# Kernel tuning notes

Measured on AMD Instinct MI355X. Metric: run time of the kernel, lower is better.

The kernel has to match this reference:

```python
import math
import jax, jax.numpy as jnp
import numpy as np

B, L, H, E = 16, 2048, 8, 64
FACTOR = 1


def setup_inputs() -> dict:
    key = jax.random.key(0)
    kq, kk, kv = jax.random.split(key, 3)
    queries = jax.random.normal(kq, (B, L, H, E), dtype=jnp.float32)
    keys = jax.random.normal(kk, (B, L, H, E), dtype=jnp.float32)
    values = jax.random.normal(kv, (B, L, H, E), dtype=jnp.float32)
    return {"queries": queries, "keys": keys, "values": values, "attn_mask": 0}


def reference(queries, keys, values, attn_mask):
    # queries/keys/values: [B, L, H, E]; attn_mask is unused (as in the original).
    b, l, h, e = queries.shape
    # [B, H, E, L]
    qp = jnp.transpose(queries, (0, 2, 3, 1))
    kp = jnp.transpose(keys, (0, 2, 3, 1))
    vp = jnp.transpose(values, (0, 2, 3, 1))

    # Period-based dependency discovery via FFT cross-correlation.
    qf = jnp.fft.rfft(qp, axis=-1)
    kf = jnp.fft.rfft(kp, axis=-1)
    corr = jnp.fft.irfft(qf * jnp.conj(kf), n=l, axis=-1)  # [B, H, E, L]

    # Inference-style time-delay aggregation (per-batch top-k delays).
    top_k = max(1, int(FACTOR * math.log(l)))
    mean_value = corr.mean(axis=(1, 2))  # [B, L]
    weights, delay = jax.lax.top_k(mean_value, top_k)  # [B, K]
    tmp_corr = jax.nn.softmax(weights, axis=-1)  # [B, K]

    # Gather from doubled tensor == circular roll: index (t + delay) mod L.
    idx = (jnp.arange(l)[None, None, :] + delay[:, :, None]) % l  # [B, K, L]
    # vp[:, None]: [B, 1, H, E, L]; idx broadcast to [B, K, 1, 1, L]
    pattern = jnp.take_along_axis(vp[:, None], idx[:, :, None, None, :], axis=-1)  # [B, K, H, E, L]
    agg = jnp.einsum('bkhel,bk->bhel', pattern, tmp_corr)  # [B, H, E, L]

    return jnp.transpose(agg, (0, 3, 1, 2))  # [B, L, H, E]
```

## Files before the change

### kernel.cpp

```cpp
#include <hip/hip_runtime.h>
#include <hip/hip_fp16.h>
#include <cstdint>
#include <cstddef>

#define BB 16
#define LL 2048
#define CC 512
#define TK 7
#define PDC(a) ((a) + ((a) >> 4))
#define PSTR 1056

typedef float2 cf;
typedef __attribute__((ext_vector_type(4))) float f32x4v;

__device__ inline cf cadd(cf a, cf b){ return make_float2(a.x + b.x, a.y + b.y); }
__device__ inline cf csub(cf a, cf b){ return make_float2(a.x - b.x, a.y - b.y); }
__device__ inline cf cmul(cf a, cf b){ return make_float2(a.x*b.x - a.y*b.y, a.x*b.y + a.y*b.x); }

template<int S> __device__ inline cf crot(cf z){
  return (S < 0) ? make_float2(z.y, -z.x) : make_float2(-z.y, z.x);
}

template<int S> __device__ inline void dft4(cf* x){
  const cf t0 = cadd(x[0], x[2]), t1 = csub(x[0], x[2]);
  const cf t2 = cadd(x[1], x[3]), t3 = csub(x[1], x[3]);
  const cf r = crot<S>(t3);
  x[0] = cadd(t0, t2); x[2] = csub(t0, t2);
  x[1] = cadd(t1, r);  x[3] = csub(t1, r);
}

template<int S> __device__ inline void dft8(cf* x){
  cf e[4] = { x[0], x[2], x[4], x[6] };
  cf o[4] = { x[1], x[3], x[5], x[7] };
  dft4<S>(e); dft4<S>(o);
  const float H = 0.70710678118654752440f;
  o[1] = cmul(o[1], make_float2(H, (float)S * H));
  o[2] = crot<S>(o[2]);
  o[3] = cmul(o[3], make_float2(-H, (float)S * H));
  x[0] = cadd(e[0], o[0]); x[4] = csub(e[0], o[0]);
  x[1] = cadd(e[1], o[1]); x[5] = csub(e[1], o[1]);
  x[2] = cadd(e[2], o[2]); x[6] = csub(e[2], o[2]);
  x[3] = cadd(e[3], o[3]); x[7] = csub(e[3], o[3]);
}

struct Tw { cf w2[7], w3[7], w4a[3], w4b[3]; };

template<int S>
__device__ inline void make_tw(int tid, Tw& T){
  const float base = (float)S * 6.283185307179586f / 2048.0f;
  const int j7 = tid & 7, j63 = tid & 63;
#pragma unroll
  for (int i = 0; i < 7; ++i){
    float s, c;
    __sincosf(base * (float)(32 * (i + 1) * j7), &s, &c);  T.w2[i] = make_float2(c, s);
    __sincosf(base * (float)( 4 * (i + 1) * j63), &s, &c); T.w3[i] = make_float2(c, s);
  }
#pragma unroll
  for (int i = 0; i < 3; ++i){
    float s, c;
    __sincosf(base * (float)((i + 1) * tid), &s, &c);         T.w4a[i] = make_float2(c, s);
    __sincosf(base * (float)((i + 1) * (tid + 256)), &s, &c); T.w4b[i] = make_float2(c, s);
  }
}

template<int S>
__device__ inline void fft_s123(cf* x, cf* Bc, cf* Cc, const Tw& T, int tid){
  dft8<S>(x);
#pragma unroll
  for (int t = 0; t < 8; ++t) Bc[PDC((tid << 3) + t)] = x[t];
  __syncthreads();
  {
    cf y[8];
#pragma unroll
    for (int t = 0; t < 8; ++t) y[t] = Bc[PDC(tid + (t << 8))];
#pragma unroll
    for (int t = 1; t < 8; ++t) y[t] = cmul(y[t], T.w2[t - 1]);
    dft8<S>(y);
    const int base = ((tid >> 3) << 6) + (tid & 7);
#pragma unroll
    for (int t = 0; t < 8; ++t) Cc[PDC(base + (t << 3))] = y[t];
  }
  __syncthreads();
  {
    cf y[8];
#pragma unroll
    for (int t = 0; t < 8; ++t) y[t] = Cc[PDC(tid + (t << 8))];
#pragma unroll
    for (int t = 1; t < 8; ++t) y[t] = cmul(y[t], T.w3[t - 1]);
    dft8<S>(y);
    const int base = ((tid >> 6) << 9) + (tid & 63);
#pragma unroll
    for (int t = 0; t < 8; ++t) Bc[PDC(base + (t << 6))] = y[t];
  }
  __syncthreads();
}

__global__ __launch_bounds__(256) void transpose_pack(const float* __restrict__ q,
                                                      const float* __restrict__ k,
                                                      __half2* __restrict__ z){
  int bid = blockIdx.x;
  const int tt = bid & 31; bid >>= 5;
  const int ct = bid & 7;  bid >>= 3;
  const int b = bid;
  const int t0 = tt << 6, c0 = ct << 6;
  __shared__ __half2 T[64][69];
  const int tid = threadIdx.x;
  const size_t inbase = ((size_t)b * LL + t0) * CC + c0;
  const int c4 = (tid & 15) << 2;
  f32x4v a[4], e[4];
#pragma unroll
  for (int p2 = 0; p2 < 4; ++p2){
    const int row = (p2 << 4) + (tid >> 4);
    a[p2] = __builtin_nontemporal_load(
        reinterpret_cast<const f32x4v*>(q + inbase + (size_t)row * CC + c4));
    e[p2] = __builtin_nontemporal_load(
        reinterpret_cast<const f32x4v*>(k + inbase + (size_t)row * CC + c4));
  }
#pragma unroll
  for (int p2 = 0; p2 < 4; ++p2){
    const int row = (p2 << 4) + (tid >> 4);
    T[row][c4 + 0] = __floats2half2_rn(a[p2][0], e[p2][0]);
    T[row][c4 + 1] = __floats2half2_rn(a[p2][1], e[p2][1]);
    T[row][c4 + 2] = __floats2half2_rn(a[p2][2], e[p2][2]);
    T[row][c4 + 3] = __floats2half2_rn(a[p2][3], e[p2][3]);
  }
  __syncthreads();
  const size_t outbase = ((size_t)b * CC + c0) * LL + (size_t)t0;
#pragma unroll
  for (int it = 0; it < 4; ++it){
    const int idx = (it << 8) + tid;
    const int c = idx >> 4;
    const int t4 = (idx & 15) << 2;
    const __half2 u0 = T[t4 + 0][c], u1 = T[t4 + 1][c];
    const __half2 u2 = T[t4 + 2][c], u3 = T[t4 + 3][c];
    uint4 w;
    w.x = *reinterpret_cast<const uint*>(&u0);
    w.y = *reinterpret_cast<const uint*>(&u1);
    w.z = *reinterpret_cast<const uint*>(&u2);
    w.w = *reinterpret_cast<const uint*>(&u3);
    *reinterpret_cast<uint4*>(&z[outbase + (size_t)c * LL + t4]) = w;
  }
}

__global__ __launch_bounds__(256) void fft_fwd(const __half2* __restrict__ z,
                                               float2* __restrict__ Ppart){
  int bid = blockIdx.x;
  const int g = bid & 63; const int b = bid >> 6;
  const int tid = threadIdx.x;
  __shared__ cf Bc[2176];
  __shared__ cf Cc[2176];
  Tw T; make_tw<-1>(tid, T);
  const __half2* zg = z + (((size_t)b * CC + (size_t)g * 8) << 11);
  float accRe[4] = {0,0,0,0};
  float accIm[4] = {0,0,0,0};
  float acc1024 = 0.f;
  __half2 h[8];
#pragma unroll
  for (int t = 0; t < 8; ++t) h[t] = zg[tid + (t << 8)];
  for (int ch = 0; ch < 8; ++ch){
    cf x[8];
#pragma unroll
    for (int t = 0; t < 8; ++t) x[t] = __half22float2(h[t]);
    if (ch < 7){
      const __half2* zn = zg + ((size_t)(ch + 1) << 11);
#pragma unroll
      for (int t = 0; t < 8; ++t) h[t] = zn[tid + (t << 8)];
    }
    fft_s123<-1>(x, Bc, Cc, T, tid);
    cf y0[4], y1[4];
#pragma unroll
    for (int t = 0; t < 4; ++t) y0[t] = Bc[PDC(tid + (t << 9))];
#pragma unroll
    for (int t = 0; t < 4; ++t) y1[t] = Bc[PDC(tid + 256 + (t << 9))];
#pragma unroll
    for (int t = 1; t < 4; ++t){
      y0[t] = cmul(y0[t], T.w4a[t - 1]);
      y1[t] = cmul(y1[t], T.w4b[t - 1]);
    }
    dft4<-1>(y0); dft4<-1>(y1);
#pragma unroll
    for (int t = 0; t < 4; ++t) Cc[PDC(tid + (t << 9))] = y0[t];
#pragma unroll
    for (int t = 0; t < 4; ++t) Cc[PDC(tid + 256 + (t << 9))] = y1[t];
    __syncthreads();
    const cf Areg[4] = { y0[0], y1[0], y0[1], y1[1] };
#pragma unroll
    for (int r = 0; r < 4; ++r){
      const int f = tid + (r << 8);
      const int p = (2048 - f) & 2047;
      const cf A = Areg[r];
      const cf Bv = Cc[PDC(p)];
      accRe[r] += 0.5f  * (Bv.y * A.x + Bv.x * A.y);
      accIm[r] += 0.25f * (A.x * A.x + A.y * A.y - Bv.x * Bv.x - Bv.y * Bv.y);
    }
    if (tid == 0){
      const cf A = y0[2];
      acc1024 += A.x * A.y;
    }
  }
  float2* pp = Ppart + ((size_t)b * 64 + g) * PSTR;
#pragma unroll
  for (int r = 0; r < 4; ++r)
    pp[tid + (r << 8)] = make_float2(accRe[r], accIm[r]);
  if (tid == 0) pp[1024] = make_float2(acc1024, 0.f);
}

__global__ __launch_bounds__(256) void reduce_P(const float2* __restrict__ Ppart,
                                                float2* __restrict__ P){
  const int gid = blockIdx.x * 256 + threadIdx.x;
  const int b = gid >> 11, f = gid & 2047;
  const int src = (f <= 1024) ? f : 2048 - f;
  const float sgn = (f <= 1024) ? 1.f : -1.f;
  float sr = 0.f, si = 0.f;
#pragma unroll 8
  for (int g = 0; g < 64; ++g){
    const float2 v = Ppart[((size_t)b * 64 + g) * PSTR + src];
    sr += v.x; si += v.y;
  }
  P[((size_t)b << 11) + f] = make_float2(sr, sgn * si);
}

__global__ __launch_bounds__(256) void fft_inv_topk(const float2* __restrict__ P,
                                                    int* __restrict__ delays,
                                                    float* __restrict__ probs){
  const int b = blockIdx.x;
  const int tid = threadIdx.x;
  __shared__ cf Bc[2176];
  __shared__ cf Cc[2176];
  __shared__ float vals[2048];
  __shared__ float rv[256]; __shared__ int ri[256];
  __shared__ float wsel[TK]; __shared__ int dsel[TK];
  Tw T; make_tw<1>(tid, T);
  cf x[8];
#pragma unroll
  for (int t = 0; t < 8; ++t) x[t] = P[((size_t)b << 11) + tid + (t << 8)];
  fft_s123<1>(x, Bc, Cc, T, tid);
  const float scale = 1.0f / (2048.0f * 512.0f);
  {
#pragma unroll
    for (int hh = 0; hh < 2; ++hh){
      const int j = tid + (hh << 8);
      cf y[4];
#pragma unroll
      for (int t = 0; t < 4; ++t) y[t] = Bc[PDC(j + (t << 9))];
      const cf* w = hh ? T.w4b : T.w4a;
#pragma unroll
      for (int t = 1; t < 4; ++t) y[t] = cmul(y[t], w[t - 1]);
      dft4<1>(y);
#pragma unroll
      for (int t = 0; t < 4; ++t) vals[j + (t << 9)] = y[t].x * scale;
    }
  }
  __syncthreads();
  for (int kk = 0; kk < TK; ++kk){
    float best = -1e30f; int bi = LL;
    for (int i = tid; i < LL; i += 256){
      const float xv = vals[i];
      if (xv > best){ best = xv; bi = i; }
    }
    rv[tid] = best; ri[tid] = bi;
    __syncthreads();
    for (int s = 128; s > 0; s >>= 1){
      if (tid < s){
        const float ov = rv[tid + s]; const int oi = ri[tid + s];
        if (ov > rv[tid] || (ov == rv[tid] && oi < ri[tid])){ rv[tid] = ov; ri[tid] = oi; }
      }
      __syncthreads();
    }
    if (tid == 0){ wsel[kk] = rv[0]; dsel[kk] = ri[0]; vals[ri[0]] = -1e30f; }
    __syncthreads();
  }
  if (tid == 0){
    const float m = wsel[0];
    float e[TK], ssum = 0.f;
#pragma unroll
    for (int i = 0; i < TK; ++i){ e[i] = expf(wsel[i] - m); ssum += e[i]; }
    const float inv = 1.0f / ssum;
#pragma unroll
    for (int i = 0; i < TK; ++i){
      probs[b * TK + i] = e[i] * inv;
      delays[b * TK + i] = dsel[i];
    }
  }
}

__global__ __launch_bounds__(256) void agg_out(const float* __restrict__ v,
                                               const int* __restrict__ delays,
                                               const float* __restrict__ probs,
                                               float* __restrict__ out){
  const int bid = blockIdx.x;
  const int xcd = bid & 7;
  const int w = bid >> 3;
  const int b = (xcd << 1) + (w >> 9);
  const int local = w & 511;
  const int tid = threadIdx.x;
  const int t = (local << 2) + (tid >> 6);
  const int i0 = tid & 63;
  const int row = (b << 11) + t;
  f32x4v acc0 = {0.f, 0.f, 0.f, 0.f};
  f32x4v acc1 = {0.f, 0.f, 0.f, 0.f};
#pragma unroll
  for (int kk = 0; kk < TK; ++kk){
    const int d = delays[b * TK + kk];
    const float p = probs[b * TK + kk];
    const int srcr = (t + d) & (LL - 1);
    const size_t base = (size_t)((b << 11) + srcr) * 128;
    const f32x4v x0 = reinterpret_cast<const f32x4v*>(v)[base + i0];
    const f32x4v x1 = reinterpret_cast<const f32x4v*>(v)[base + i0 + 64];
    acc0 += x0 * p;
    acc1 += x1 * p;
  }
  f32x4v* o = reinterpret_cast<f32x4v*>(out) + (size_t)row * 128;
  o[i0] = acc0;
  o[i0 + 64] = acc1;
}

extern "C" void kernel_launch(void* const* d_in, const int* in_sizes, int n_in,
                              void* d_out, int out_size, void* d_ws, size_t ws_size,
                              hipStream_t stream){
  const float* q = (const float*)d_in[0];
  const float* k = (const float*)d_in[1];
  const float* v = (const float*)d_in[2];
  float* out = (float*)d_out;

  char* ws = (char*)d_ws;
  const size_t Z_BYTES  = (size_t)BB * CC * LL * sizeof(__half2);
  const size_t PP_BYTES = (size_t)BB * 64 * PSTR * sizeof(float2);
  const size_t P_BYTES  = (size_t)BB * LL * sizeof(float2);
  __half2* zbuf = (__half2*)ws;
  float2* Ppart = (float2*)(ws + Z_BYTES);
  float2* Pbuf  = (float2*)(ws + Z_BYTES + PP_BYTES);
  int* delays = (int*)(ws + Z_BYTES + PP_BYTES + P_BYTES);
  float* probs = (float*)(ws + Z_BYTES + PP_BYTES + P_BYTES + 1024);

  hipLaunchKernelGGL(transpose_pack, dim3(BB * 32 * 8), dim3(256), 0, stream, q, k, zbuf);
  hipLaunchKernelGGL(fft_fwd, dim3(BB * 64), dim3(256), 0, stream, zbuf, Ppart);
  hipLaunchKernelGGL(reduce_P, dim3((BB * LL) / 256), dim3(256), 0, stream, Ppart, Pbuf);
  hipLaunchKernelGGL(fft_inv_topk, dim3(BB), dim3(256), 0, stream, Pbuf, delays, probs);
  hipLaunchKernelGGL(agg_out, dim3(BB * 512), dim3(256), 0, stream,
                     v, delays, probs, out);
}
```

Before: 121.0 us.

## Split forward FFT across more blocks with single shared buffer; batch agg loads

The forward FFT kernel now launches twice as many blocks, each handling 4 channel pairs instead of 8, and uses one shared-memory buffer instead of two. This adds extra barriers so the buffer can be reused safely. The partial-sum buffer and the reduce kernel are widened to match. The aggregation kernel issues all seven gathered loads before accumulating and writes its output with nontemporal stores. The aim is more occupancy and memory-level parallelism, at the cost of a larger partial-sum reduction and more synchronisation.

```diff
diff --git a/kernel.cpp b/kernel.cpp
--- a/kernel.cpp
+++ b/kernel.cpp
@@ -9,6 +9,7 @@
 #define TK 7
 #define PDC(a) ((a) + ((a) >> 4))
 #define PSTR 1056
+#define NG 128
 
 typedef float2 cf;
 typedef __attribute__((ext_vector_type(4))) float f32x4v;
@@ -64,7 +65,7 @@
 }
 
 template<int S>
-__device__ inline void fft_s123(cf* x, cf* Bc, cf* Cc, const Tw& T, int tid){
+__device__ inline void fft_s123(cf* Bc, cf* Cc, cf* x, const Tw& T, int tid){
   dft8<S>(x);
 #pragma unroll
   for (int t = 0; t < 8; ++t) Bc[PDC((tid << 3) + t)] = x[t];
@@ -145,33 +146,61 @@
 __global__ __launch_bounds__(256) void fft_fwd(const __half2* __restrict__ z,
                                                float2* __restrict__ Ppart){
   int bid = blockIdx.x;
-  const int g = bid & 63; const int b = bid >> 6;
+  const int g = bid & (NG - 1); const int b = bid >> 7;
   const int tid = threadIdx.x;
-  __shared__ cf Bc[2176];
-  __shared__ cf Cc[2176];
+  __shared__ cf B[2176];
   Tw T; make_tw<-1>(tid, T);
-  const __half2* zg = z + (((size_t)b * CC + (size_t)g * 8) << 11);
+  const __half2* zg = z + (((size_t)b * CC + (size_t)g * 4) << 11);
   float accRe[4] = {0,0,0,0};
   float accIm[4] = {0,0,0,0};
   float acc1024 = 0.f;
   __half2 h[8];
 #pragma unroll
   for (int t = 0; t < 8; ++t) h[t] = zg[tid + (t << 8)];
-  for (int ch = 0; ch < 8; ++ch){
+  for (int ch = 0; ch < 4; ++ch){
     cf x[8];
 #pragma unroll
     for (int t = 0; t < 8; ++t) x[t] = __half22float2(h[t]);
-    if (ch < 7){
+    if (ch < 3){
       const __half2* zn = zg + ((size_t)(ch + 1) << 11);
 #pragma unroll
       for (int t = 0; t < 8; ++t) h[t] = zn[tid + (t << 8)];
     }
-    fft_s123<-1>(x, Bc, Cc, T, tid);
+    dft8<-1>(x);
+    __syncthreads();
+#pragma unroll
+    for (int t = 0; t < 8; ++t) B[PDC((tid << 3) + t)] = x[t];
+    __syncthreads();
+    cf y[8];
+#pragma unroll
+    for (int t = 0; t < 8; ++t) y[t] = B[PDC(tid + (t << 8))];
+#pragma unroll
+    for (int t = 1; t < 8; ++t) y[t] = cmul(y[t], T.w2[t - 1]);
+    dft8<-1>(y);
+    __syncthreads();
+    {
+      const int base = ((tid >> 3) << 6) + (tid & 7);
+#pragma unroll
+      for (int t = 0; t < 8; ++t) B[PDC(base + (t << 3))] = y[t];
+    }
+    __syncthreads();
+#pragma unroll
+    for (int t = 0; t < 8; ++t) y[t] = B[PDC(tid + (t << 8))];
+#pragma unroll
+    for (int t = 1; t < 8; ++t) y[t] = cmul(y[t], T.w3[t - 1]);
+    dft8<-1>(y);
+    __syncthreads();
+    {
+      const int base = ((tid >> 6) << 9) + (tid & 63);
+#pragma unroll
+      for (int t = 0; t < 8; ++t) B[PDC(base + (t << 6))] = y[t];
+    }
+    __syncthreads();
     cf y0[4], y1[4];
 #pragma unroll
-    for (int t = 0; t < 4; ++t) y0[t] = Bc[PDC(tid + (t << 9))];
-#pragma unroll
-    for (int t = 0; t < 4; ++t) y1[t] = Bc[PDC(tid + 256 + (t << 9))];
+    for (int t = 0; t < 4; ++t) y0[t] = B[PDC(tid + (t << 9))];
+#pragma unroll
+    for (int t = 0; t < 4; ++t) y1[t] = B[PDC(tid + 256 + (t << 9))];
 #pragma unroll
     for (int t = 1; t < 4; ++t){
       y0[t] = cmul(y0[t], T.w4a[t - 1]);
@@ -179,9 +208,9 @@
     }
     dft4<-1>(y0); dft4<-1>(y1);
 #pragma unroll
-    for (int t = 0; t < 4; ++t) Cc[PDC(tid + (t << 9))] = y0[t];
-#pragma unroll
-    for (int t = 0; t < 4; ++t) Cc[PDC(tid + 256 + (t << 9))] = y1[t];
+    for (int t = 0; t < 4; ++t) B[PDC(tid + (t << 9))] = y0[t];
+#pragma unroll
+    for (int t = 0; t < 4; ++t) B[PDC(tid + 256 + (t << 9))] = y1[t];
     __syncthreads();
     const cf Areg[4] = { y0[0], y1[0], y0[1], y1[1] };
 #pragma unroll
@@ -189,7 +218,7 @@
       const int f = tid + (r << 8);
       const int p = (2048 - f) & 2047;
       const cf A = Areg[r];
-      const cf Bv = Cc[PDC(p)];
+      const cf Bv = B[PDC(p)];
       accRe[r] += 0.5f  * (Bv.y * A.x + Bv.x * A.y);
       accIm[r] += 0.25f * (A.x * A.x + A.y * A.y - Bv.x * Bv.x - Bv.y * Bv.y);
     }
@@ -198,7 +227,7 @@
       acc1024 += A.x * A.y;
     }
   }
-  float2* pp = Ppart + ((size_t)b * 64 + g) * PSTR;
+  float2* pp = Ppart + ((size_t)b * NG + g) * PSTR;
 #pragma unroll
   for (int r = 0; r < 4; ++r)
     pp[tid + (r << 8)] = make_float2(accRe[r], accIm[r]);
@@ -213,8 +242,8 @@
   const float sgn = (f <= 1024) ? 1.f : -1.f;
   float sr = 0.f, si = 0.f;
 #pragma unroll 8
-  for (int g = 0; g < 64; ++g){
-    const float2 v = Ppart[((size_t)b * 64 + g) * PSTR + src];
+  for (int g = 0; g < NG; ++g){
+    const float2 v = Ppart[((size_t)b * NG + g) * PSTR + src];
     sr += v.x; si += v.y;
   }
   P[((size_t)b << 11) + f] = make_float2(sr, sgn * si);
@@ -234,7 +263,7 @@
   cf x[8];
 #pragma unroll
   for (int t = 0; t < 8; ++t) x[t] = P[((size_t)b << 11) + tid + (t << 8)];
-  fft_s123<1>(x, Bc, Cc, T, tid);
+  fft_s123<1>(Bc, Cc, x, T, tid);
   const float scale = 1.0f / (2048.0f * 512.0f);
   {
 #pragma unroll
@@ -297,22 +326,31 @@
   const int t = (local << 2) + (tid >> 6);
   const int i0 = tid & 63;
   const int row = (b << 11) + t;
+  float p[TK]; int d[TK];
+#pragma unroll
+  for (int kk = 0; kk < TK; ++kk){
+    d[kk] = delays[b * TK + kk];
+    p[kk] = probs[b * TK + kk];
+  }
+  const f32x4v* v4 = reinterpret_cast<const f32x4v*>(v);
+  f32x4v x0[TK], x1[TK];
+#pragma unroll
+  for (int kk = 0; kk < TK; ++kk){
+    const int srcr = (t + d[kk]) & (LL - 1);
+    const size_t base = (size_t)((b << 11) + srcr) * 128;
+    x0[kk] = v4[base + i0];
+    x1[kk] = v4[base + i0 + 64];
+  }
   f32x4v acc0 = {0.f, 0.f, 0.f, 0.f};
   f32x4v acc1 = {0.f, 0.f, 0.f, 0.f};
 #pragma unroll
   for (int kk = 0; kk < TK; ++kk){
-    const int d = delays[b * TK + kk];
-    const float p = probs[b * TK + kk];
-    const int srcr = (t + d) & (LL - 1);
-    const size_t base = (size_t)((b << 11) + srcr) * 128;
-    const f32x4v x0 = reinterpret_cast<const f32x4v*>(v)[base + i0];
-    const f32x4v x1 = reinterpret_cast<const f32x4v*>(v)[base + i0 + 64];
-    acc0 += x0 * p;
-    acc1 += x1 * p;
+    acc0 += x0[kk] * p[kk];
+    acc1 += x1[kk] * p[kk];
   }
   f32x4v* o = reinterpret_cast<f32x4v*>(out) + (size_t)row * 128;
-  o[i0] = acc0;
-  o[i0 + 64] = acc1;
+  __builtin_nontemporal_store(acc0, o + i0);
+  __builtin_nontemporal_store(acc1, o + i0 + 64);
 }
 
 extern "C" void kernel_launch(void* const* d_in, const int* in_sizes, int n_in,
@@ -325,7 +363,7 @@
 
   char* ws = (char*)d_ws;
   const size_t Z_BYTES  = (size_t)BB * CC * LL * sizeof(__half2);
-  const size_t PP_BYTES = (size_t)BB * 64 * PSTR * sizeof(float2);
+  const size_t PP_BYTES = (size_t)BB * NG * PSTR * sizeof(float2);
   const size_t P_BYTES  = (size_t)BB * LL * sizeof(float2);
   __half2* zbuf = (__half2*)ws;
   float2* Ppart = (float2*)(ws + Z_BYTES);
@@ -334,7 +372,7 @@
   float* probs = (float*)(ws + Z_BYTES + PP_BYTES + P_BYTES + 1024);
 
   hipLaunchKernelGGL(transpose_pack, dim3(BB * 32 * 8), dim3(256), 0, stream, q, k, zbuf);
-  hipLaunchKernelGGL(fft_fwd, dim3(BB * 64), dim3(256), 0, stream, zbuf, Ppart);
+  hipLaunchKernelGGL(fft_fwd, dim3(BB * NG), dim3(256), 0, stream, zbuf, Ppart);
   hipLaunchKernelGGL(reduce_P, dim3((BB * LL) / 256), dim3(256), 0, stream, Ppart, Pbuf);
   hipLaunchKernelGGL(fft_inv_topk, dim3(BB), dim3(256), 0, stream, Pbuf, delays, probs);
   hipLaunchKernelGGL(agg_out, dim3(BB * 512), dim3(256), 0, stream,
```

Measured after the change: 115.9 us. -4.2%, faster.
